# Optimization experiments

Measured on AMD Instinct MI355X. Metric: run time of the kernel, lower is better.

## Reference

```python
import jax, jax.numpy as jnp
import numpy as np

R, TR = 47, 2  # response_size, treat_size


def _lstm_cell(x, h, c, Wih, Whh, bih, bhh):
    # PyTorch gate order: i, f, g, o
    gates = x @ Wih.T + h @ Whh.T + bih + bhh
    i, f, g, o = jnp.split(gates, 4, axis=-1)
    c_new = jax.nn.sigmoid(f) * c + jax.nn.sigmoid(i) * jnp.tanh(g)
    h_new = jax.nn.sigmoid(o) * jnp.tanh(c_new)
    return h_new, c_new


def setup_inputs() -> dict:
    key = jax.random.key(0)
    B, T = 256, 2048
    ks = jax.random.split(key, 20)

    def u(k, shape, H):
        s = 1.0 / np.sqrt(H).astype(np.float32)
        return jax.random.uniform(k, shape, jnp.float32, -s, s)

    return {
        "x_r": jax.random.normal(ks[0], (B, T, R), jnp.float32),
        "x_t": jax.random.normal(ks[1], (B, T, TR), jnp.float32),
        # r_rnn: 2-layer LSTM, input 49 -> hidden 47
        "r_Wih0": u(ks[2], (4 * R, R + TR), R), "r_Whh0": u(ks[3], (4 * R, R), R),
        "r_bih0": u(ks[4], (4 * R,), R), "r_bhh0": u(ks[5], (4 * R,), R),
        "r_Wih1": u(ks[6], (4 * R, R), R), "r_Whh1": u(ks[7], (4 * R, R), R),
        "r_bih1": u(ks[8], (4 * R,), R), "r_bhh1": u(ks[9], (4 * R,), R),
        # t_rnn: 2-layer LSTM, input 96 -> hidden 2
        "t_Wih0": u(ks[10], (4 * TR, 2 * R + TR), TR), "t_Whh0": u(ks[11], (4 * TR, TR), TR),
        "t_bih0": u(ks[12], (4 * TR,), TR), "t_bhh0": u(ks[13], (4 * TR,), TR),
        "t_Wih1": u(ks[14], (4 * TR, TR), TR), "t_Whh1": u(ks[15], (4 * TR, TR), TR),
        "t_bih1": u(ks[16], (4 * TR,), TR), "t_bhh1": u(ks[17], (4 * TR,), TR),
    }


def reference(x_r, x_t,
              r_Wih0, r_Whh0, r_bih0, r_bhh0, r_Wih1, r_Whh1, r_bih1, r_bhh1,
              t_Wih0, t_Whh0, t_bih0, t_bhh0, t_Wih1, t_Whh1, t_bih1, t_bhh1):
    B = x_r.shape[0]
    zR = jnp.zeros((B, R), x_r.dtype)
    zT = jnp.zeros((B, TR), x_r.dtype)

    def step(carry, xs):
        hr0, cr0, hr1, cr1, ht0, ct0, ht1, ct1 = carry
        r, t = xs  # [B,47], [B,2]
        r_in = jnp.concatenate([r, t], axis=-1)              # [B,49]
        hr0, cr0 = _lstm_cell(r_in, hr0, cr0, r_Wih0, r_Whh0, r_bih0, r_bhh0)
        hr1, cr1 = _lstm_cell(hr0, hr1, cr1, r_Wih1, r_Whh1, r_bih1, r_bhh1)
        t_in = jnp.concatenate([r_in, hr1], axis=-1)         # [B,96]
        ht0, ct0 = _lstm_cell(t_in, ht0, ct0, t_Wih0, t_Whh0, t_bih0, t_bhh0)
        ht1, ct1 = _lstm_cell(ht0, ht1, ct1, t_Wih1, t_Whh1, t_bih1, t_bhh1)
        return (hr0, cr0, hr1, cr1, ht0, ct0, ht1, ct1), (hr1, ht1)

    init = (zR, zR, zR, zR, zT, zT, zT, zT)
    xs = (x_r.transpose(1, 0, 2), x_t.transpose(1, 0, 2))    # time-major
    _, (r_seq, t_seq) = jax.lax.scan(step, init, xs)         # [T,B,47], [T,B,2]
    return (r_seq.transpose(1, 0, 2), t_seq.transpose(1, 0, 2))
```

## Files before the change

### kernel.cpp

```cpp
#include <hip/hip_runtime.h>

#define T_STEPS 2048
#define TOTAL   2064

typedef float f2 __attribute__((ext_vector_type(2)));
typedef _Float16 h2 __attribute__((ext_vector_type(2)));

__device__ __forceinline__ float fast_rcp(float x) { return __builtin_amdgcn_rcpf(x); }
__device__ __forceinline__ float sig_f(float x) { return fast_rcp(1.0f + __expf(-x)); }
__device__ __forceinline__ float tanh_f(float x) {
    float e = __expf(-2.0f * x);
    return fmaf(2.0f, fast_rcp(1.0f + e), -1.0f);
}
__device__ __forceinline__ float gate_act(float x, float zm, float sm, float sa) {
    float e = __expf(-x * zm);
    return fmaf(fast_rcp(1.0f + e), sm, sa);
}

#if __has_builtin(__builtin_amdgcn_fdot2)
#define FDOT2(a, b, c) __builtin_amdgcn_fdot2((a), (b), (c), false)
#else
__device__ __forceinline__ float FDOT2(h2 a, h2 b, float c) {
    return fmaf((float)a.x, (float)b.x, fmaf((float)a.y, (float)b.y, c));
}
#endif

#define LDS_BARRIER() asm volatile("s_waitcnt lgkmcnt(0)\n\ts_barrier" ::: "memory")

#define DPP_BCAST0 0x00
#define DPP_BCAST1 0x55
#define DPP_BCAST2 0xAA
#define DPP_BCAST3 0xFF
#define DPP_PAIR   0xF5
#define DPP_ROR4   0x124
#define DPP_ROR8   0x128
template<int CTRL>
__device__ __forceinline__ float dppf(float x) {
    int r = __builtin_amdgcn_update_dpp(0, __builtin_bit_cast(int, x), CTRL, 0xF, 0xF, true);
    return __builtin_bit_cast(float, r);
}

__device__ __forceinline__ h2 pk16(float a, float b) {
    return __builtin_bit_cast(h2, __builtin_amdgcn_cvt_pkrtz(a, b));
}

__device__ __forceinline__ void unpackh(h2 (&in)[24], const h2* __restrict__ row) {
    const float4* q = (const float4*)row;
#pragma unroll
    for (int k = 0; k < 6; ++k) {
        float4 v = q[k];
        in[4 * k + 0] = __builtin_bit_cast(h2, v.x);
        in[4 * k + 1] = __builtin_bit_cast(h2, v.y);
        in[4 * k + 2] = __builtin_bit_cast(h2, v.z);
        in[4 * k + 3] = __builtin_bit_cast(h2, v.w);
    }
}
__device__ __forceinline__ void unpackx(h2 (&in)[28], const h2* __restrict__ row) {
    const float4* q = (const float4*)row;
#pragma unroll
    for (int k = 0; k < 7; ++k) {
        float4 v = q[k];
        in[4 * k + 0] = __builtin_bit_cast(h2, v.x);
        in[4 * k + 1] = __builtin_bit_cast(h2, v.y);
        in[4 * k + 2] = __builtin_bit_cast(h2, v.z);
        in[4 * k + 3] = __builtin_bit_cast(h2, v.w);
    }
}

__device__ __forceinline__ void loadw47h(h2 (&w)[24], const float* __restrict__ src) {
#pragma unroll
    for (int u = 0; u < 23; ++u)
        w[u] = h2{(_Float16)src[2 * u], (_Float16)src[2 * u + 1]};
    w[23] = h2{(_Float16)src[46], (_Float16)0.0f};
}
__device__ __forceinline__ void loadw49h(h2 (&w)[25], const float* __restrict__ src) {
#pragma unroll
    for (int u = 0; u < 24; ++u)
        w[u] = h2{(_Float16)src[2 * u], (_Float16)src[2 * u + 1]};
    w[24] = h2{(_Float16)src[48], (_Float16)0.0f};
}

__device__ __forceinline__ void loadx4c(float (&dst)[4], const float* __restrict__ x_r,
                                        const float* __restrict__ x_t,
                                        size_t xrb, size_t xtb, int k) {
#pragma unroll
    for (int m = 0; m < 4; ++m) {
        int v = 4 * k + m;
        dst[m] = (v < 47) ? x_r[xrb + v] : ((v < 49) ? x_t[xtb + (v - 47)] : 0.0f);
    }
}

__global__ __launch_bounds__(192) void adrnn_fused(
    const float* __restrict__ x_r, const float* __restrict__ x_t,
    const float* __restrict__ rWih0, const float* __restrict__ rWhh0,
    const float* __restrict__ rbih0, const float* __restrict__ rbhh0,
    const float* __restrict__ rWih1, const float* __restrict__ rWhh1,
    const float* __restrict__ rbih1, const float* __restrict__ rbhh1,
    const float* __restrict__ tWih0, const float* __restrict__ tWhh0,
    const float* __restrict__ tbih0, const float* __restrict__ tbhh0,
    const float* __restrict__ tWih1, const float* __restrict__ tWhh1,
    const float* __restrict__ tbih1, const float* __restrict__ tbhh1,
    float* __restrict__ r_out, float* __restrict__ t_out)
{
    __shared__ __align__(16) h2 xring[32][28];
    __shared__ __align__(16) h2 h0f16[16][24];
    __shared__ __align__(16) h2 h1f16[16][24];

    const int tid = threadIdx.x;
    const int wid = tid >> 6;
    const int l   = tid & 63;
    const int j   = l;
    const int b = blockIdx.x;
    const size_t xr_base = (size_t)b * T_STEPS * 47;
    const size_t xt_base = (size_t)b * T_STEPS * 2;

    for (int k = tid; k < 16 * 24; k += 192) {
        h0f16[k / 24][k % 24] = h2{(_Float16)0.0f, (_Float16)0.0f};
        h1f16[k / 24][k % 24] = h2{(_Float16)0.0f, (_Float16)0.0f};
    }

    if (wid == 0) {
        h2 wx[4][25]; h2 wh[4][24]; float bias[4] = {0, 0, 0, 0};
#pragma unroll
        for (int g = 0; g < 4; ++g) {
#pragma unroll
            for (int u = 0; u < 25; ++u) wx[g][u] = h2{(_Float16)0.0f, (_Float16)0.0f};
#pragma unroll
            for (int u = 0; u < 24; ++u) wh[g][u] = h2{(_Float16)0.0f, (_Float16)0.0f};
        }
        if (j < 47) {
#pragma unroll
            for (int g = 0; g < 4; ++g) {
                const int row = g * 47 + j;
                loadw49h(wx[g], &rWih0[row * 49]);
                loadw47h(wh[g], &rWhh0[row * 47]);
                bias[g] = rbih0[row] + rbhh0[row];
            }
        }
        float c0 = 0.f;
        __syncthreads();
        for (int i = 0; i < TOTAL; ++i) {
            float hv = 0.0f;
            if (i < T_STEPS && j < 47) {
                h2 xin[28];
                unpackx(xin, &xring[i & 31][0]);
                h2 hin[24];
                unpackh(hin, &h0f16[(i - 1) & 15][0]);
                float a0 = bias[0], a1 = bias[1], a2 = bias[2], a3 = bias[3];
#pragma unroll
                for (int u = 0; u < 25; ++u) {
                    a0 = FDOT2(wx[0][u], xin[u], a0);
                    a1 = FDOT2(wx[1][u], xin[u], a1);
                    a2 = FDOT2(wx[2][u], xin[u], a2);
                    a3 = FDOT2(wx[3][u], xin[u], a3);
                }
#pragma unroll
                for (int u = 0; u < 24; ++u) {
                    a0 = FDOT2(wh[0][u], hin[u], a0);
                    a1 = FDOT2(wh[1][u], hin[u], a1);
                    a2 = FDOT2(wh[2][u], hin[u], a2);
                    a3 = FDOT2(wh[3][u], hin[u], a3);
                }
                float iv = sig_f(a0), fv = sig_f(a1);
                float gv = tanh_f(a2), ov = sig_f(a3);
                c0 = fmaf(fv, c0, iv * gv);
                hv = ov * tanh_f(c0);
            }
            float hn = dppf<DPP_PAIR>(hv);
            if (i < T_STEPS && j < 47 && !(j & 1)) h0f16[i & 15][j >> 1] = pk16(hv, hn);
            if ((i & 7) == 7) LDS_BARRIER();
        }
    } else if (wid == 1) {
        h2 wx[4][24]; h2 wh[4][24]; float bias[4] = {0, 0, 0, 0};
#pragma unroll
        for (int g = 0; g < 4; ++g) {
#pragma unroll
            for (int u = 0; u < 24; ++u) {
                wx[g][u] = h2{(_Float16)0.0f, (_Float16)0.0f};
                wh[g][u] = h2{(_Float16)0.0f, (_Float16)0.0f};
            }
        }
        if (j < 47) {
#pragma unroll
            for (int g = 0; g < 4; ++g) {
                const int row = g * 47 + j;
                loadw47h(wx[g], &rWih1[row * 47]);
                loadw47h(wh[g], &rWhh1[row * 47]);
                bias[g] = rbih1[row] + rbhh1[row];
            }
        }
        float c1 = 0.f;
        __syncthreads();
        for (int i = 0; i < TOTAL; ++i) {
            const int s = i - 8;
            float hv = 0.0f;
            if (s >= 0 && s < T_STEPS && j < 47) {
                h2 xin[24];
                unpackh(xin, &h0f16[s & 15][0]);
                h2 hin[24];
                unpackh(hin, &h1f16[(s - 1) & 15][0]);
                float a0 = bias[0], a1 = bias[1], a2 = bias[2], a3 = bias[3];
#pragma unroll
                for (int u = 0; u < 24; ++u) {
                    a0 = FDOT2(wx[0][u], xin[u], a0);
                    a1 = FDOT2(wx[1][u], xin[u], a1);
                    a2 = FDOT2(wx[2][u], xin[u], a2);
                    a3 = FDOT2(wx[3][u], xin[u], a3);
                }
#pragma unroll
                for (int u = 0; u < 24; ++u) {
                    a0 = FDOT2(wh[0][u], hin[u], a0);
                    a1 = FDOT2(wh[1][u], hin[u], a1);
                    a2 = FDOT2(wh[2][u], hin[u], a2);
                    a3 = FDOT2(wh[3][u], hin[u], a3);
                }
                float iv = sig_f(a0), fv = sig_f(a1);
                float gv = tanh_f(a2), ov = sig_f(a3);
                c1 = fmaf(fv, c1, iv * gv);
                hv = ov * tanh_f(c1);
                r_out[((size_t)b * T_STEPS + s) * 47 + j] = hv;
            }
            float hn = dppf<DPP_PAIR>(hv);
            if (s >= 0 && s < T_STEPS && j < 47 && !(j & 1)) h1f16[s & 15][j >> 1] = pk16(hv, hn);
            if ((i & 7) == 7) LDS_BARRIER();
        }
    } else {
        const int tu  = (l >> 2) & 1;
        const int tg  = l & 3;
        const int thf = (l >> 3) & 1;
        const int R0 = tg * 2 + tu;
        h2 wt[24]; float wx48;
        if (thf == 0) {
            wx48 = 0.f;
#pragma unroll
            for (int u = 0; u < 24; ++u)
                wt[u] = h2{(_Float16)tWih0[R0 * 96 + 2 * u], (_Float16)tWih0[R0 * 96 + 2 * u + 1]};
        } else {
            wx48 = tWih0[R0 * 96 + 48];
#pragma unroll
            for (int u = 0; u < 23; ++u)
                wt[u] = h2{(_Float16)tWih0[R0 * 96 + 49 + 2 * u], (_Float16)tWih0[R0 * 96 + 49 + 2 * u + 1]};
            wt[23] = h2{(_Float16)tWih0[R0 * 96 + 95], (_Float16)0.0f};
        }
        const float bT0 = tbih0[R0] + tbhh0[R0];
        const float wh00 = tWhh0[R0 * 2 + 0], wh01 = tWhh0[R0 * 2 + 1];
        const float wi10 = tWih1[R0 * 2 + 0], wi11 = tWih1[R0 * 2 + 1];
        const float wh10 = tWhh1[R0 * 2 + 0], wh11 = tWhh1[R0 * 2 + 1];
        const float bT1 = tbih1[R0] + tbhh1[R0];
        const bool isg = (tg == 2);
        const float zm = isg ? 2.f : 1.f, sm = isg ? 2.f : 1.f, sa = isg ? -1.f : 0.f;
        float ht00 = 0.f, ht01 = 0.f, ct0u = 0.f;
        float ht10 = 0.f, ht11 = 0.f, ct1u = 0.f;

        float xa[4] = {0,0,0,0}, xb[4] = {0,0,0,0}, xc[4] = {0,0,0,0};
        if (l < 13) {
            for (int t = 0; t < 8; ++t) {
                float xv[4];
                loadx4c(xv, x_r, x_t, xr_base + (size_t)t * 47, xt_base + (size_t)t * 2, l);
                xring[t][2 * l]     = pk16(xv[0], xv[1]);
                xring[t][2 * l + 1] = pk16(xv[2], xv[3]);
            }
            loadx4c(xa, x_r, x_t, xr_base + (size_t)8 * 47,  xt_base + (size_t)8 * 2,  l);
            loadx4c(xb, x_r, x_t, xr_base + (size_t)9 * 47,  xt_base + (size_t)9 * 2,  l);
            loadx4c(xc, x_r, x_t, xr_base + (size_t)10 * 47, xt_base + (size_t)10 * 2, l);
        }
        __syncthreads();

        for (int i = 0; i < TOTAL; ++i) {
            if (l < 13) {
                const int tw = i + 8;
                if (tw < T_STEPS) {
                    xring[tw & 31][2 * l]     = pk16(xa[0], xa[1]);
                    xring[tw & 31][2 * l + 1] = pk16(xa[2], xa[3]);
                }
#pragma unroll
                for (int m = 0; m < 4; ++m) { xa[m] = xb[m]; xb[m] = xc[m]; }
                int tl = i + 11;
                if (tl > T_STEPS - 1) tl = T_STEPS - 1;
                loadx4c(xc, x_r, x_t, xr_base + (size_t)tl * 47, xt_base + (size_t)tl * 2, l);
            }
            const int s = i - 16;
            if (s >= 0 && s < T_STEPS) {
                const h2* src = (thf == 0) ? &xring[s & 31][0] : &h1f16[s & 15][0];
                h2 tin[24];
                unpackh(tin, src);
                float x48v = (float)xring[s & 31][24].x;
                float acc = 0.f;
#pragma unroll
                for (int u = 0; u < 24; ++u) acc = FDOT2(wt[u], tin[u], acc);
                float part = (thf == 1) ? fmaf(wx48, x48v, acc) : acc;
                float pre0 = part + dppf<DPP_ROR8>(part);
                pre0 += bT0 + wh00 * ht00 + wh01 * ht01;
                float a0 = gate_act(pre0, zm, sm, sa);
                float i0 = dppf<DPP_BCAST0>(a0);
                float f0 = dppf<DPP_BCAST1>(a0);
                float g0 = dppf<DPP_BCAST2>(a0);
                float o0 = dppf<DPP_BCAST3>(a0);
                ct0u = fmaf(f0, ct0u, i0 * g0);
                float htu = o0 * tanh_f(ct0u);
                float hto = dppf<DPP_ROR4>(htu);
                ht00 = (tu == 0) ? htu : hto;
                ht01 = (tu == 0) ? hto : htu;
                float pre1 = bT1 + wi10 * ht00 + wi11 * ht01 + wh10 * ht10 + wh11 * ht11;
                float a1 = gate_act(pre1, zm, sm, sa);
                float ji = dppf<DPP_BCAST0>(a1);
                float jf = dppf<DPP_BCAST1>(a1);
                float jg = dppf<DPP_BCAST2>(a1);
                float jo = dppf<DPP_BCAST3>(a1);
                ct1u = fmaf(jf, ct1u, ji * jg);
                float h1u = jo * tanh_f(ct1u);
                float h1o = dppf<DPP_ROR4>(h1u);
                ht10 = (tu == 0) ? h1u : h1o;
                ht11 = (tu == 0) ? h1o : h1u;
                if (l == 0) {
                    float2 tv = {ht10, ht11};
                    *reinterpret_cast<float2*>(&t_out[((size_t)b * T_STEPS + s) * 2]) = tv;
                }
            }
            if ((i & 7) == 7) LDS_BARRIER();
        }
    }
}

extern "C" void kernel_launch(void* const* d_in, const int* in_sizes, int n_in,
                              void* d_out, int out_size, void* d_ws, size_t ws_size,
                              hipStream_t stream) {
    const float* x_r   = (const float*)d_in[0];
    const float* x_t   = (const float*)d_in[1];
    const float* rWih0 = (const float*)d_in[2];
    const float* rWhh0 = (const float*)d_in[3];
    const float* rbih0 = (const float*)d_in[4];
    const float* rbhh0 = (const float*)d_in[5];
    const float* rWih1 = (const float*)d_in[6];
    const float* rWhh1 = (const float*)d_in[7];
    const float* rbih1 = (const float*)d_in[8];
    const float* rbhh1 = (const float*)d_in[9];
    const float* tWih0 = (const float*)d_in[10];
    const float* tWhh0 = (const float*)d_in[11];
    const float* tbih0 = (const float*)d_in[12];
    const float* tbhh0 = (const float*)d_in[13];
    const float* tWih1 = (const float*)d_in[14];
    const float* tWhh1 = (const float*)d_in[15];
    const float* tbih1 = (const float*)d_in[16];
    const float* tbhh1 = (const float*)d_in[17];

    float* r_out = (float*)d_out;
    float* t_out = r_out + (size_t)256 * T_STEPS * 47;

    hipLaunchKernelGGL(adrnn_fused, dim3(256), dim3(192), 0, stream,
                       x_r, x_t, rWih0, rWhh0, rbih0, rbhh0, rWih1, rWhh1, rbih1, rbhh1,
                       tWih0, tWhh0, tbih0, tbhh0, tWih1, tWhh1, tbih1, tbhh1,
                       r_out, t_out);
}
```

Measured before the change: 1.277 ms.

## Compute r-LSTM gate matvecs with MFMA using fused h/x LDS vectors

```diff
diff --git a/kernel.cpp b/kernel.cpp
--- a/kernel.cpp
+++ b/kernel.cpp
@@ -3,8 +3,9 @@
 #define T_STEPS 2048
 #define TOTAL   2064
 
-typedef float f2 __attribute__((ext_vector_type(2)));
 typedef _Float16 h2 __attribute__((ext_vector_type(2)));
+typedef _Float16 h8 __attribute__((ext_vector_type(8)));
+typedef float    f4v __attribute__((ext_vector_type(4)));
 
 __device__ __forceinline__ float fast_rcp(float x) { return __builtin_amdgcn_rcpf(x); }
 __device__ __forceinline__ float sig_f(float x) { return fast_rcp(1.0f + __expf(-x)); }
@@ -55,38 +56,14 @@
         in[4 * k + 3] = __builtin_bit_cast(h2, v.w);
     }
 }
-__device__ __forceinline__ void unpackx(h2 (&in)[28], const h2* __restrict__ row) {
-    const float4* q = (const float4*)row;
-#pragma unroll
-    for (int k = 0; k < 7; ++k) {
-        float4 v = q[k];
-        in[4 * k + 0] = __builtin_bit_cast(h2, v.x);
-        in[4 * k + 1] = __builtin_bit_cast(h2, v.y);
-        in[4 * k + 2] = __builtin_bit_cast(h2, v.z);
-        in[4 * k + 3] = __builtin_bit_cast(h2, v.w);
-    }
-}
-
-__device__ __forceinline__ void loadw47h(h2 (&w)[24], const float* __restrict__ src) {
-#pragma unroll
-    for (int u = 0; u < 23; ++u)
-        w[u] = h2{(_Float16)src[2 * u], (_Float16)src[2 * u + 1]};
-    w[23] = h2{(_Float16)src[46], (_Float16)0.0f};
-}
-__device__ __forceinline__ void loadw49h(h2 (&w)[25], const float* __restrict__ src) {
-#pragma unroll
-    for (int u = 0; u < 24; ++u)
-        w[u] = h2{(_Float16)src[2 * u], (_Float16)src[2 * u + 1]};
-    w[24] = h2{(_Float16)src[48], (_Float16)0.0f};
-}
-
-__device__ __forceinline__ void loadx4c(float (&dst)[4], const float* __restrict__ x_r,
-                                        const float* __restrict__ x_t,
+
+__device__ __forceinline__ void loadx8c(float (&dst)[8], const float* __restrict__ xr,
+                                        const float* __restrict__ xt,
                                         size_t xrb, size_t xtb, int k) {
 #pragma unroll
-    for (int m = 0; m < 4; ++m) {
-        int v = 4 * k + m;
-        dst[m] = (v < 47) ? x_r[xrb + v] : ((v < 49) ? x_t[xtb + (v - 47)] : 0.0f);
+    for (int m = 0; m < 8; ++m) {
+        int v = 8 * k + m;
+        dst[m] = (v < 47) ? xr[xrb + v] : ((v < 49) ? xt[xtb + (v - 47)] : 0.0f);
     }
 }
 
@@ -102,9 +79,11 @@
     const float* __restrict__ tbih1, const float* __restrict__ tbhh1,
     float* __restrict__ r_out, float* __restrict__ t_out)
 {
-    __shared__ __align__(16) h2 xring[32][28];
-    __shared__ __align__(16) h2 h0f16[16][24];
-    __shared__ __align__(16) h2 h1f16[16][24];
+    __shared__ __align__(16) h2 vring0[32][64];
+    __shared__ __align__(16) h2 vring1[16][64];
+    __shared__ __align__(16) h2 t1ring[16][24];
+    __shared__ __align__(16) float gbuf0[192];
+    __shared__ __align__(16) float gbuf1[192];
 
     const int tid = threadIdx.x;
     const int wid = tid >> 6;
@@ -114,114 +93,155 @@
     const size_t xr_base = (size_t)b * T_STEPS * 47;
     const size_t xt_base = (size_t)b * T_STEPS * 2;
 
-    for (int k = tid; k < 16 * 24; k += 192) {
-        h0f16[k / 24][k % 24] = h2{(_Float16)0.0f, (_Float16)0.0f};
-        h1f16[k / 24][k % 24] = h2{(_Float16)0.0f, (_Float16)0.0f};
+    if (tid < 23) vring0[0][tid] = h2{(_Float16)0.0f, (_Float16)0.0f};
+    else if (tid == 23) ((_Float16*)&vring0[0][0])[46] = (_Float16)0.0f;
+    else if (tid >= 24 && tid < 48) vring1[0][tid - 24] = h2{(_Float16)0.0f, (_Float16)0.0f};
+    else if (tid >= 48 && tid < 64) {
+        int s = tid - 48;
+        ((_Float16*)&vring1[s][0])[47] = (_Float16)0.0f;
+        ((_Float16*)&vring1[s][0])[95] = (_Float16)0.0f;
+        ((_Float16*)&t1ring[s][0])[47] = (_Float16)0.0f;
     }
 
     if (wid == 0) {
-        h2 wx[4][25]; h2 wh[4][24]; float bias[4] = {0, 0, 0, 0};
-#pragma unroll
-        for (int g = 0; g < 4; ++g) {
-#pragma unroll
-            for (int u = 0; u < 25; ++u) wx[g][u] = h2{(_Float16)0.0f, (_Float16)0.0f};
-#pragma unroll
-            for (int u = 0; u < 24; ++u) wh[g][u] = h2{(_Float16)0.0f, (_Float16)0.0f};
-        }
+        h8 A[12][3];
+#pragma unroll
+        for (int t = 0; t < 12; ++t) {
+#pragma unroll
+            for (int kk = 0; kk < 3; ++kk) {
+                const int m = t * 16 + (l & 15);
+#pragma unroll
+                for (int e = 0; e < 8; ++e) {
+                    const int k = kk * 32 + (l >> 4) * 8 + e;
+                    float w = 0.0f;
+                    if (m < 188) {
+                        if (k < 47) w = rWhh0[m * 47 + k];
+                        else if (k == 47) w = rWih0[m * 49 + 48];
+                        else w = rWih0[m * 49 + (k - 48)];
+                    }
+                    A[t][kk][e] = (_Float16)w;
+                }
+            }
+        }
+        float b0 = 0, b1 = 0, b2 = 0, b3 = 0;
         if (j < 47) {
-#pragma unroll
-            for (int g = 0; g < 4; ++g) {
-                const int row = g * 47 + j;
-                loadw49h(wx[g], &rWih0[row * 49]);
-                loadw47h(wh[g], &rWhh0[row * 47]);
-                bias[g] = rbih0[row] + rbhh0[row];
-            }
+            b0 = rbih0[j] + rbhh0[j];
+            b1 = rbih0[47 + j] + rbhh0[47 + j];
+            b2 = rbih0[94 + j] + rbhh0[94 + j];
+            b3 = rbih0[141 + j] + rbhh0[141 + j];
         }
         float c0 = 0.f;
         __syncthreads();
         for (int i = 0; i < TOTAL; ++i) {
-            float hv = 0.0f;
-            if (i < T_STEPS && j < 47) {
-                h2 xin[28];
-                unpackx(xin, &xring[i & 31][0]);
-                h2 hin[24];
-                unpackh(hin, &h0f16[(i - 1) & 15][0]);
-                float a0 = bias[0], a1 = bias[1], a2 = bias[2], a3 = bias[3];
-#pragma unroll
-                for (int u = 0; u < 25; ++u) {
-                    a0 = FDOT2(wx[0][u], xin[u], a0);
-                    a1 = FDOT2(wx[1][u], xin[u], a1);
-                    a2 = FDOT2(wx[2][u], xin[u], a2);
-                    a3 = FDOT2(wx[3][u], xin[u], a3);
-                }
-#pragma unroll
-                for (int u = 0; u < 24; ++u) {
-                    a0 = FDOT2(wh[0][u], hin[u], a0);
-                    a1 = FDOT2(wh[1][u], hin[u], a1);
-                    a2 = FDOT2(wh[2][u], hin[u], a2);
-                    a3 = FDOT2(wh[3][u], hin[u], a3);
-                }
-                float iv = sig_f(a0), fv = sig_f(a1);
-                float gv = tanh_f(a2), ov = sig_f(a3);
-                c0 = fmaf(fv, c0, iv * gv);
-                hv = ov * tanh_f(c0);
-            }
-            float hn = dppf<DPP_PAIR>(hv);
-            if (i < T_STEPS && j < 47 && !(j & 1)) h0f16[i & 15][j >> 1] = pk16(hv, hn);
+            if (i < T_STEPS) {
+                const float4* vrow = reinterpret_cast<const float4*>(&vring0[i & 31][0]);
+                const int g4 = l >> 4;
+                h8 bf0 = __builtin_bit_cast(h8, vrow[g4]);
+                h8 bf1 = __builtin_bit_cast(h8, vrow[g4 + 4]);
+                h8 bf2 = __builtin_bit_cast(h8, vrow[g4 + 8]);
+#pragma unroll
+                for (int t = 0; t < 12; ++t) {
+                    f4v acc = {0.f, 0.f, 0.f, 0.f};
+                    acc = __builtin_amdgcn_mfma_f32_16x16x32_f16(A[t][0], bf0, acc, 0, 0, 0);
+                    acc = __builtin_amdgcn_mfma_f32_16x16x32_f16(A[t][1], bf1, acc, 0, 0, 0);
+                    acc = __builtin_amdgcn_mfma_f32_16x16x32_f16(A[t][2], bf2, acc, 0, 0, 0);
+                    if ((l & 15) == t) {
+                        float4 st = {acc[0], acc[1], acc[2], acc[3]};
+                        *reinterpret_cast<float4*>(&gbuf0[t * 16 + g4 * 4]) = st;
+                    }
+                }
+                float hv = 0.f;
+                if (j < 47) {
+                    float p0 = gbuf0[j] + b0;
+                    float p1 = gbuf0[47 + j] + b1;
+                    float p2 = gbuf0[94 + j] + b2;
+                    float p3 = gbuf0[141 + j] + b3;
+                    float iv = sig_f(p0), fv = sig_f(p1);
+                    float gv = tanh_f(p2), ov = sig_f(p3);
+                    c0 = fmaf(fv, c0, iv * gv);
+                    hv = ov * tanh_f(c0);
+                }
+                float hn = dppf<DPP_PAIR>(hv);
+                if (j < 46 && !(j & 1)) {
+                    h2 p = pk16(hv, hn);
+                    vring0[(i + 1) & 31][j >> 1] = p;
+                    vring1[i & 15][24 + (j >> 1)] = p;
+                } else if (j == 46) {
+                    ((_Float16*)&vring0[(i + 1) & 31][0])[46] = (_Float16)hv;
+                    ((_Float16*)&vring1[i & 15][0])[94] = (_Float16)hv;
+                }
+            }
             if ((i & 7) == 7) LDS_BARRIER();
         }
     } else if (wid == 1) {
-        h2 wx[4][24]; h2 wh[4][24]; float bias[4] = {0, 0, 0, 0};
-#pragma unroll
-        for (int g = 0; g < 4; ++g) {
-#pragma unroll
-            for (int u = 0; u < 24; ++u) {
-                wx[g][u] = h2{(_Float16)0.0f, (_Float16)0.0f};
-                wh[g][u] = h2{(_Float16)0.0f, (_Float16)0.0f};
-            }
-        }
+        h8 A[12][3];
+#pragma unroll
+        for (int t = 0; t < 12; ++t) {
+#pragma unroll
+            for (int kk = 0; kk < 3; ++kk) {
+                const int m = t * 16 + (l & 15);
+#pragma unroll
+                for (int e = 0; e < 8; ++e) {
+                    const int k = kk * 32 + (l >> 4) * 8 + e;
+                    float w = 0.0f;
+                    if (m < 188) {
+                        if (k < 47) w = rWhh1[m * 47 + k];
+                        else if (k >= 48 && k < 95) w = rWih1[m * 47 + (k - 48)];
+                    }
+                    A[t][kk][e] = (_Float16)w;
+                }
+            }
+        }
+        float b0 = 0, b1 = 0, b2 = 0, b3 = 0;
         if (j < 47) {
-#pragma unroll
-            for (int g = 0; g < 4; ++g) {
-                const int row = g * 47 + j;
-                loadw47h(wx[g], &rWih1[row * 47]);
-                loadw47h(wh[g], &rWhh1[row * 47]);
-                bias[g] = rbih1[row] + rbhh1[row];
-            }
+            b0 = rbih1[j] + rbhh1[j];
+            b1 = rbih1[47 + j] + rbhh1[47 + j];
+            b2 = rbih1[94 + j] + rbhh1[94 + j];
+            b3 = rbih1[141 + j] + rbhh1[141 + j];
         }
         float c1 = 0.f;
         __syncthreads();
         for (int i = 0; i < TOTAL; ++i) {
             const int s = i - 8;
-            float hv = 0.0f;
-            if (s >= 0 && s < T_STEPS && j < 47) {
-                h2 xin[24];
-                unpackh(xin, &h0f16[s & 15][0]);
-                h2 hin[24];
-                unpackh(hin, &h1f16[(s - 1) & 15][0]);
-                float a0 = bias[0], a1 = bias[1], a2 = bias[2], a3 = bias[3];
-#pragma unroll
-                for (int u = 0; u < 24; ++u) {
-                    a0 = FDOT2(wx[0][u], xin[u], a0);
-                    a1 = FDOT2(wx[1][u], xin[u], a1);
-                    a2 = FDOT2(wx[2][u], xin[u], a2);
-                    a3 = FDOT2(wx[3][u], xin[u], a3);
-                }
-#pragma unroll
-                for (int u = 0; u < 24; ++u) {
-                    a0 = FDOT2(wh[0][u], hin[u], a0);
-                    a1 = FDOT2(wh[1][u], hin[u], a1);
-                    a2 = FDOT2(wh[2][u], hin[u], a2);
-                    a3 = FDOT2(wh[3][u], hin[u], a3);
-                }
-                float iv = sig_f(a0), fv = sig_f(a1);
-                float gv = tanh_f(a2), ov = sig_f(a3);
-                c1 = fmaf(fv, c1, iv * gv);
-                hv = ov * tanh_f(c1);
-                r_out[((size_t)b * T_STEPS + s) * 47 + j] = hv;
-            }
-            float hn = dppf<DPP_PAIR>(hv);
-            if (s >= 0 && s < T_STEPS && j < 47 && !(j & 1)) h1f16[s & 15][j >> 1] = pk16(hv, hn);
+            if (s >= 0 && s < T_STEPS) {
+                const float4* vrow = reinterpret_cast<const float4*>(&vring1[s & 15][0]);
+                const int g4 = l >> 4;
+                h8 bf0 = __builtin_bit_cast(h8, vrow[g4]);
+                h8 bf1 = __builtin_bit_cast(h8, vrow[g4 + 4]);
+                h8 bf2 = __builtin_bit_cast(h8, vrow[g4 + 8]);
+#pragma unroll
+                for (int t = 0; t < 12; ++t) {
+                    f4v acc = {0.f, 0.f, 0.f, 0.f};
+                    acc = __builtin_amdgcn_mfma_f32_16x16x32_f16(A[t][0], bf0, acc, 0, 0, 0);
+                    acc = __builtin_amdgcn_mfma_f32_16x16x32_f16(A[t][1], bf1, acc, 0, 0, 0);
+                    acc = __builtin_amdgcn_mfma_f32_16x16x32_f16(A[t][2], bf2, acc, 0, 0, 0);
+                    if ((l & 15) == t) {
+                        float4 st = {acc[0], acc[1], acc[2], acc[3]};
+                        *reinterpret_cast<float4*>(&gbuf1[t * 16 + g4 * 4]) = st;
+                    }
+                }
+                float hv = 0.f;
+                if (j < 47) {
+                    float p0 = gbuf1[j] + b0;
+                    float p1 = gbuf1[47 + j] + b1;
+                    float p2 = gbuf1[94 + j] + b2;
+                    float p3 = gbuf1[141 + j] + b3;
+                    float iv = sig_f(p0), fv = sig_f(p1);
+                    float gv = tanh_f(p2), ov = sig_f(p3);
+                    c1 = fmaf(fv, c1, iv * gv);
+                    hv = ov * tanh_f(c1);
+                    r_out[((size_t)b * T_STEPS + s) * 47 + j] = hv;
+                }
+                float hn = dppf<DPP_PAIR>(hv);
+                if (j < 46 && !(j & 1)) {
+                    h2 p = pk16(hv, hn);
+                    vring1[(s + 1) & 15][j >> 1] = p;
+                    t1ring[s & 15][j >> 1] = p;
+                } else if (j == 46) {
+                    ((_Float16*)&vring1[(s + 1) & 15][0])[46] = (_Float16)hv;
+                    ((_Float16*)&t1ring[s & 15][0])[46] = (_Float16)hv;
+                }
+            }
             if ((i & 7) == 7) LDS_BARRIER();
         }
     } else {
@@ -252,39 +272,49 @@
         float ht00 = 0.f, ht01 = 0.f, ct0u = 0.f;
         float ht10 = 0.f, ht11 = 0.f, ct1u = 0.f;
 
-        float xa[4] = {0,0,0,0}, xb[4] = {0,0,0,0}, xc[4] = {0,0,0,0};
-        if (l < 13) {
+        float xa[8] = {0,0,0,0,0,0,0,0}, xb[8] = {0,0,0,0,0,0,0,0}, xc[8] = {0,0,0,0,0,0,0,0};
+        if (l < 7) {
             for (int t = 0; t < 8; ++t) {
-                float xv[4];
-                loadx4c(xv, x_r, x_t, xr_base + (size_t)t * 47, xt_base + (size_t)t * 2, l);
-                xring[t][2 * l]     = pk16(xv[0], xv[1]);
-                xring[t][2 * l + 1] = pk16(xv[2], xv[3]);
-            }
-            loadx4c(xa, x_r, x_t, xr_base + (size_t)8 * 47,  xt_base + (size_t)8 * 2,  l);
-            loadx4c(xb, x_r, x_t, xr_base + (size_t)9 * 47,  xt_base + (size_t)9 * 2,  l);
-            loadx4c(xc, x_r, x_t, xr_base + (size_t)10 * 47, xt_base + (size_t)10 * 2, l);
+                float xv[8];
+                loadx8c(xv, x_r, x_t, xr_base + (size_t)t * 47, xt_base + (size_t)t * 2, l);
+                if (l < 6) {
+                    h2* d = &vring0[t][24 + 4 * l];
+                    d[0] = pk16(xv[0], xv[1]); d[1] = pk16(xv[2], xv[3]);
+                    d[2] = pk16(xv[4], xv[5]); d[3] = pk16(xv[6], xv[7]);
+                } else {
+                    ((_Float16*)&vring0[t][0])[47] = (_Float16)xv[0];
+                }
+            }
+            loadx8c(xa, x_r, x_t, xr_base + (size_t)8 * 47,  xt_base + (size_t)8 * 2,  l);
+            loadx8c(xb, x_r, x_t, xr_base + (size_t)9 * 47,  xt_base + (size_t)9 * 2,  l);
+            loadx8c(xc, x_r, x_t, xr_base + (size_t)10 * 47, xt_base + (size_t)10 * 2, l);
         }
         __syncthreads();
 
         for (int i = 0; i < TOTAL; ++i) {
-            if (l < 13) {
+            if (l < 7) {
                 const int tw = i + 8;
                 if (tw < T_STEPS) {
-                    xring[tw & 31][2 * l]     = pk16(xa[0], xa[1]);
-                    xring[tw & 31][2 * l + 1] = pk16(xa[2], xa[3]);
-                }
-#pragma unroll
-                for (int m = 0; m < 4; ++m) { xa[m] = xb[m]; xb[m] = xc[m]; }
+                    if (l < 6) {
+                        h2* d = &vring0[tw & 31][24 + 4 * l];
+                        d[0] = pk16(xa[0], xa[1]); d[1] = pk16(xa[2], xa[3]);
+                        d[2] = pk16(xa[4], xa[5]); d[3] = pk16(xa[6], xa[7]);
+                    } else {
+                        ((_Float16*)&vring0[tw & 31][0])[47] = (_Float16)xa[0];
+                    }
+                }
+#pragma unroll
+                for (int m = 0; m < 8; ++m) { xa[m] = xb[m]; xb[m] = xc[m]; }
                 int tl = i + 11;
                 if (tl > T_STEPS - 1) tl = T_STEPS - 1;
-                loadx4c(xc, x_r, x_t, xr_base + (size_t)tl * 47, xt_base + (size_t)tl * 2, l);
+                loadx8c(xc, x_r, x_t, xr_base + (size_t)tl * 47, xt_base + (size_t)tl * 2, l);
             }
             const int s = i - 16;
             if (s >= 0 && s < T_STEPS) {
-                const h2* src = (thf == 0) ? &xring[s & 31][0] : &h1f16[s & 15][0];
+                const h2* src = (thf == 0) ? &vring0[s & 31][24] : &t1ring[s & 15][0];
                 h2 tin[24];
                 unpackh(tin, src);
-                float x48v = (float)xring[s & 31][24].x;
+                float x48v = (float)((const _Float16*)&vring0[s & 31][0])[47];
                 float acc = 0.f;
 #pragma unroll
                 for (int u = 0; u < 24; ++u) acc = FDOT2(wt[u], tin[u], acc);
@@ -294,9 +324,9 @@
                 float a0 = gate_act(pre0, zm, sm, sa);
                 float i0 = dppf<DPP_BCAST0>(a0);
                 float f0 = dppf<DPP_BCAST1>(a0);
-                float g0 = dppf<DPP_BCAST2>(a0);
+                float g0v = dppf<DPP_BCAST2>(a0);
                 float o0 = dppf<DPP_BCAST3>(a0);
-                ct0u = fmaf(f0, ct0u, i0 * g0);
+                ct0u = fmaf(f0, ct0u, i0 * g0v);
                 float htu = o0 * tanh_f(ct0u);
                 float hto = dppf<DPP_ROR4>(htu);
                 ht00 = (tu == 0) ? htu : hto;
```

Result: slower. 1.793 ms (+40.4%).
